# Optimization experiments

Measured on AMD Instinct MI355X. Metric: run time of the kernel, lower is better.

The kernel has to match this reference:

```python
import jax, jax.numpy as jnp
import numpy as np

VOCAB_SIZE = 32000
BOS_ID = 1
BSZ, SEQLEN = 8, 2048


def setup_inputs() -> dict:
    key = jax.random.key(0)
    input_ids = jax.random.randint(key, (BSZ, SEQLEN), 0, VOCAB_SIZE, dtype=jnp.int64 if jax.config.jax_enable_x64 else jnp.int32)
    return {"input_ids": input_ids}


def reference(input_ids) -> jnp.ndarray:
    bsz, seqlen = input_ids.shape
    # valid tokens: exclude pad (0) and BOS
    valid = (input_ids != 0) & (input_ids != BOS_ID)  # [B, S] bool
    # batched histogram: counts[b, v] = # of valid occurrences of v in row b
    counts = jnp.zeros((bsz, VOCAB_SIZE), dtype=jnp.int32)
    counts = counts.at[jnp.arange(bsz)[:, None], input_ids].add(valid.astype(jnp.int32))
    # majority token per row (argmax ties -> lowest index, same as torch)
    pred = jnp.argmax(counts, axis=1)  # [B]
    # rows with no valid tokens fall back to BOS_ID
    pred = jnp.where(valid.any(axis=1), pred, BOS_ID)  # [B]
    # logits: -6 everywhere, +6 at pred column for every position
    vocab_ids = jnp.arange(VOCAB_SIZE)  # [V]
    logits = jnp.where(
        vocab_ids[None, None, :] == pred[:, None, None],
        jnp.float32(6.0),
        jnp.float32(-6.0),
    )  # [B, 1, V] -> broadcast to [B, S, V]
    return jnp.broadcast_to(logits, (bsz, seqlen, VOCAB_SIZE))
```

## Files before the change

kernel.cpp:

```cpp
#include <hip/hip_runtime.h>

#define VOCAB   32000
#define BSZ     8
#define SEQLEN  2048
#define BOS_ID  1

__global__ void wm_zero_counts(int* __restrict__ counts) {
    int i = blockIdx.x * blockDim.x + threadIdx.x;
    if (i < BSZ * VOCAB) counts[i] = 0;
}

__global__ void wm_histogram(const int* __restrict__ ids, int* __restrict__ counts) {
    const int b = blockIdx.x;
    const int* row = ids + b * SEQLEN;
    int* cnt = counts + b * VOCAB;
    for (int s = threadIdx.x; s < SEQLEN; s += blockDim.x) {
        int t = row[s];
        if (t != 0 && t != BOS_ID) atomicAdd(&cnt[t], 1);
    }
}

__global__ void wm_argmax(const int* __restrict__ counts, int* __restrict__ pred) {
    const int b = blockIdx.x;
    const int* cnt = counts + b * VOCAB;

    int best_c = 0;
    int best_i = VOCAB;
    for (int v = threadIdx.x; v < VOCAB; v += blockDim.x) {
        int c = cnt[v];
        if (c > best_c || (c == best_c && v < best_i)) { best_c = c; best_i = v; }
    }

    __shared__ int sc[256];
    __shared__ int si[256];
    sc[threadIdx.x] = best_c;
    si[threadIdx.x] = best_i;
    __syncthreads();
    for (int off = 128; off > 0; off >>= 1) {
        if ((int)threadIdx.x < off) {
            int c2 = sc[threadIdx.x + off];
            int i2 = si[threadIdx.x + off];
            if (c2 > sc[threadIdx.x] || (c2 == sc[threadIdx.x] && i2 < si[threadIdx.x])) {
                sc[threadIdx.x] = c2;
                si[threadIdx.x] = i2;
            }
        }
        __syncthreads();
    }
    if (threadIdx.x == 0) {
        pred[b] = (sc[0] == 0) ? BOS_ID : si[0];
    }
}

__global__ void wm_fill(float4* __restrict__ out, long long n4) {
    long long i = (long long)blockIdx.x * blockDim.x + threadIdx.x;
    const long long stride = (long long)gridDim.x * blockDim.x;
    const float4 val = make_float4(-6.0f, -6.0f, -6.0f, -6.0f);
    for (; i < n4; i += stride) out[i] = val;
}

__global__ void wm_spike(float* __restrict__ out, const int* __restrict__ pred) {
    int i = blockIdx.x * blockDim.x + threadIdx.x;
    if (i < BSZ * SEQLEN) {
        int b = i / SEQLEN;
        out[(long long)i * VOCAB + pred[b]] = 6.0f;
    }
}

extern "C" void kernel_launch(void* const* d_in, const int* in_sizes, int n_in,
                              void* d_out, int out_size, void* d_ws, size_t ws_size,
                              hipStream_t stream) {
    const int* ids = (const int*)d_in[0];
    float* out = (float*)d_out;

    int* counts = (int*)d_ws;
    int* pred   = counts + BSZ * VOCAB;

    {
        int n = BSZ * VOCAB;
        wm_zero_counts<<<(n + 255) / 256, 256, 0, stream>>>(counts);
    }
    wm_histogram<<<BSZ, 256, 0, stream>>>(ids, counts);
    wm_argmax<<<BSZ, 256, 0, stream>>>(counts, pred);
    {
        const long long n4 = (long long)BSZ * SEQLEN * VOCAB / 4;
        wm_fill<<<32768, 256, 0, stream>>>((float4*)out, n4);
    }
    {
        int n = BSZ * SEQLEN;
        wm_spike<<<(n + 255) / 256, 256, 0, stream>>>(out, pred);
    }
}
```

Baseline: 2.098 ms.

## Fuse histogram/argmax in LDS and fuse fill with spike using nontemporal stores

Replaces five kernels with two. The histogram is built in shared memory with two 16-bit counters packed per word, and the argmax runs in the same block, so there is no global count buffer to zero and no extra launches. The fill kernel writes each output row once with the spike folded in, using nontemporal stores, instead of a full fill followed by a scattered spike pass. The 16-bit counters cannot overflow here because a row holds at most 2048 tokens.

```diff
diff --git a/kernel.cpp b/kernel.cpp
--- a/kernel.cpp
+++ b/kernel.cpp
@@ -4,66 +4,76 @@
 #define BSZ     8
 #define SEQLEN  2048
 #define BOS_ID  1
+#define HWORDS  (VOCAB / 2)
+#define ROW4    (VOCAB / 4)
 
-__global__ void wm_zero_counts(int* __restrict__ counts) {
-    int i = blockIdx.x * blockDim.x + threadIdx.x;
-    if (i < BSZ * VOCAB) counts[i] = 0;
-}
+typedef float f32x4 __attribute__((ext_vector_type(4)));
 
-__global__ void wm_histogram(const int* __restrict__ ids, int* __restrict__ counts) {
-    const int b = blockIdx.x;
+__global__ __launch_bounds__(1024)
+void wm_predict(const int* __restrict__ ids, int* __restrict__ pred) {
+    __shared__ unsigned cnt[HWORDS];
+    const int b   = blockIdx.x;
+    const int tid = threadIdx.x;
+
+    for (int i = tid; i < HWORDS; i += 1024) cnt[i] = 0;
+    __syncthreads();
+
     const int* row = ids + b * SEQLEN;
-    int* cnt = counts + b * VOCAB;
-    for (int s = threadIdx.x; s < SEQLEN; s += blockDim.x) {
+    for (int s = tid; s < SEQLEN; s += 1024) {
         int t = row[s];
-        if (t != 0 && t != BOS_ID) atomicAdd(&cnt[t], 1);
+        if (t > BOS_ID)
+            atomicAdd(&cnt[t >> 1], 1u << ((t & 1) << 4));
     }
-}
-
-__global__ void wm_argmax(const int* __restrict__ counts, int* __restrict__ pred) {
-    const int b = blockIdx.x;
-    const int* cnt = counts + b * VOCAB;
+    __syncthreads();
 
     int best_c = 0;
     int best_i = VOCAB;
-    for (int v = threadIdx.x; v < VOCAB; v += blockDim.x) {
-        int c = cnt[v];
-        if (c > best_c || (c == best_c && v < best_i)) { best_c = c; best_i = v; }
+    for (int w = tid; w < HWORDS; w += 1024) {
+        unsigned x = cnt[w];
+        int c0 = (int)(x & 0xffffu);
+        int c1 = (int)(x >> 16);
+        if (c0 > best_c) { best_c = c0; best_i = 2 * w; }
+        if (c1 > best_c) { best_c = c1; best_i = 2 * w + 1; }
     }
+    __syncthreads();
 
-    __shared__ int sc[256];
-    __shared__ int si[256];
-    sc[threadIdx.x] = best_c;
-    si[threadIdx.x] = best_i;
+    int* sc = (int*)cnt;
+    int* si = sc + 1024;
+    sc[tid] = best_c;
+    si[tid] = best_i;
     __syncthreads();
-    for (int off = 128; off > 0; off >>= 1) {
-        if ((int)threadIdx.x < off) {
-            int c2 = sc[threadIdx.x + off];
-            int i2 = si[threadIdx.x + off];
-            if (c2 > sc[threadIdx.x] || (c2 == sc[threadIdx.x] && i2 < si[threadIdx.x])) {
-                sc[threadIdx.x] = c2;
-                si[threadIdx.x] = i2;
+    for (int off = 512; off > 0; off >>= 1) {
+        if (tid < off) {
+            int c2 = sc[tid + off];
+            int i2 = si[tid + off];
+            if (c2 > sc[tid] || (c2 == sc[tid] && i2 < si[tid])) {
+                sc[tid] = c2;
+                si[tid] = i2;
             }
         }
         __syncthreads();
     }
-    if (threadIdx.x == 0) {
-        pred[b] = (sc[0] == 0) ? BOS_ID : si[0];
-    }
+    if (tid == 0) pred[b] = (sc[0] == 0) ? BOS_ID : si[0];
 }
 
-__global__ void wm_fill(float4* __restrict__ out, long long n4) {
-    long long i = (long long)blockIdx.x * blockDim.x + threadIdx.x;
-    const long long stride = (long long)gridDim.x * blockDim.x;
-    const float4 val = make_float4(-6.0f, -6.0f, -6.0f, -6.0f);
-    for (; i < n4; i += stride) out[i] = val;
-}
+__global__ __launch_bounds__(256)
+void wm_fill_spike(f32x4* __restrict__ out, const int* __restrict__ pred) {
+    const int r  = blockIdx.x;
+    const int p  = pred[r >> 11];
+    const int p4 = p >> 2;
+    f32x4* row = out + (long long)r * ROW4;
 
-__global__ void wm_spike(float* __restrict__ out, const int* __restrict__ pred) {
-    int i = blockIdx.x * blockDim.x + threadIdx.x;
-    if (i < BSZ * SEQLEN) {
-        int b = i / SEQLEN;
-        out[(long long)i * VOCAB + pred[b]] = 6.0f;
+    const f32x4 neg = { -6.0f, -6.0f, -6.0f, -6.0f };
+    f32x4 spike;
+    spike[0] = ((p & 3) == 0) ? 6.0f : -6.0f;
+    spike[1] = ((p & 3) == 1) ? 6.0f : -6.0f;
+    spike[2] = ((p & 3) == 2) ? 6.0f : -6.0f;
+    spike[3] = ((p & 3) == 3) ? 6.0f : -6.0f;
+
+    #pragma unroll 4
+    for (int j = threadIdx.x; j < ROW4; j += 256) {
+        f32x4 v = (j == p4) ? spike : neg;
+        __builtin_nontemporal_store(v, row + j);
     }
 }
 
@@ -71,23 +81,9 @@
                               void* d_out, int out_size, void* d_ws, size_t ws_size,
                               hipStream_t stream) {
     const int* ids = (const int*)d_in[0];
-    float* out = (float*)d_out;
+    f32x4* out = (f32x4*)d_out;
+    int* pred = (int*)d_ws;
 
-    int* counts = (int*)d_ws;
-    int* pred   = counts + BSZ * VOCAB;
-
-    {
-        int n = BSZ * VOCAB;
-        wm_zero_counts<<<(n + 255) / 256, 256, 0, stream>>>(counts);
-    }
-    wm_histogram<<<BSZ, 256, 0, stream>>>(ids, counts);
-    wm_argmax<<<BSZ, 256, 0, stream>>>(counts, pred);
-    {
-        const long long n4 = (long long)BSZ * SEQLEN * VOCAB / 4;
-        wm_fill<<<32768, 256, 0, stream>>>((float4*)out, n4);
-    }
-    {
-        int n = BSZ * SEQLEN;
-        wm_spike<<<(n + 255) / 256, 256, 0, stream>>>(out, pred);
-    }
+    wm_predict<<<BSZ, 1024, 0, stream>>>(ids, pred);
+    wm_fill_spike<<<BSZ * SEQLEN, 256, 0, stream>>>(out, pred);
 }
```

After: 2.057 ms. Within noise of the previous version (-1.9%).
